# Kernel optimization log

Hardware: AMD Instinct MI355X
Metric: run time of the kernel (lower is better)

## Reference

```python
import jax, jax.numpy as jnp
import numpy as np

B, S, D = 2, 2048, 1024
H, HD = 16, 64
WINDOW = 256
THETA = 10000.0
SCALING = 1.0


def _rope_tables(seq_len, dim, dtype):
    # Matches RotaryEmbedding: inv_freq over even indices, emb = cat((freqs, freqs), -1)
    inv_freq = 1.0 / (THETA ** (jnp.arange(0, dim, 2, dtype=jnp.float32) / dim))
    t = jnp.arange(seq_len, dtype=jnp.float32) / max(SCALING, 1e-6)
    freqs = jnp.outer(t, inv_freq)                      # [S, HD/2]
    emb = jnp.concatenate((freqs, freqs), axis=-1)      # [S, HD]
    return jnp.cos(emb).astype(dtype), jnp.sin(emb).astype(dtype)


def _rotate_half(x):
    # interleaved-pair rotation, faithful to the torch code
    x1 = x[..., ::2]
    x2 = x[..., 1::2]
    return jnp.stack((-x2, x1), axis=-1).reshape(x.shape)


def setup_inputs() -> dict:
    key = jax.random.key(0)
    ks = jax.random.split(key, 5)
    x = jax.random.normal(ks[0], (B, S, D), dtype=jnp.float32)
    w = lambda k: (jax.random.normal(k, (D, D), dtype=jnp.float32) * 0.02)
    return {"x": x, "Wq": w(ks[1]), "Wk": w(ks[2]), "Wv": w(ks[3]), "Wo": w(ks[4])}


def reference(x, Wq, Wk, Wv, Wo):
    bsz, seq_len, d_model = x.shape
    # QKV projections (torch Linear: y = x @ W.T), reshape to [B, H, S, HD]
    def proj(W):
        return (x @ W.T).reshape(bsz, seq_len, H, HD).transpose(0, 2, 1, 3)
    q, k, v = proj(Wq), proj(Wk), proj(Wv)

    cos, sin = _rope_tables(seq_len, HD, x.dtype)       # [S, HD]
    cos = cos[None, None]                               # [1,1,S,HD]
    sin = sin[None, None]
    q = q * cos + _rotate_half(q) * sin
    k = k * cos + _rotate_half(k) * sin

    scale = 1.0 / jnp.sqrt(jnp.asarray(HD, dtype=x.dtype))
    scores = jnp.einsum('bhqd,bhkd->bhqk', q, k) * scale  # [B,H,S,S]

    idx = jnp.arange(seq_len)
    allow = (idx[:, None] >= idx[None, :]) & (idx[:, None] - idx[None, :] < WINDOW)
    neg = jnp.asarray(jnp.finfo(scores.dtype).min, dtype=scores.dtype)
    scores = jnp.where(allow[None, None], scores, neg)

    attn = jax.nn.softmax(scores, axis=-1)
    y = jnp.einsum('bhqk,bhkd->bhqd', attn, v)           # [B,H,S,HD]
    y = y.transpose(0, 2, 1, 3).reshape(bsz, seq_len, d_model)
    return y @ Wo.T
```

## Files before the change

### kernel.cpp

```cpp
#include <hip/hip_runtime.h>
#include <math.h>
#include <stdint.h>

typedef unsigned short u16;
typedef __bf16 bf16x8 __attribute__((ext_vector_type(8)));
typedef float f32x4 __attribute__((ext_vector_type(4)));

constexpr int Bb = 2, Ss = 2048, Dd = 1024, Hh = 16, Hd = 64, Win = 256;
constexpr int Mtot = Bb * Ss;

__device__ __forceinline__ u16 f2bf(float f) {
    uint32_t u = __float_as_uint(f);
    u += 0x7fff + ((u >> 16) & 1);
    return (u16)(u >> 16);
}

__device__ __forceinline__ void gload16(const void* g, void* l) {
    __builtin_amdgcn_global_load_lds(
        (const __attribute__((address_space(1))) uint32_t*)g,
        (__attribute__((address_space(3))) uint32_t*)l, 16, 0, 0);
}

__global__ void prep(const float* __restrict__ x,
                     const float* __restrict__ Wq, const float* __restrict__ Wk,
                     const float* __restrict__ Wv, const float* __restrict__ Wo,
                     u16* __restrict__ xb,
                     u16* __restrict__ wqb, u16* __restrict__ wkb,
                     u16* __restrict__ wvb, u16* __restrict__ wob,
                     float2* __restrict__ cs) {
    const int bid = blockIdx.x;
    if (bid < 8192) {
        const float* s;
        u16* d;
        int i;
        if (bid < 4096) {
            s = x; d = xb; i = bid * 256 + threadIdx.x;
        } else {
            int wsel = (bid - 4096) >> 10;
            i = ((bid - 4096) & 1023) * 256 + threadIdx.x;
            s = (wsel == 0) ? Wq : (wsel == 1) ? Wk : (wsel == 2) ? Wv : Wo;
            d = (wsel == 0) ? wqb : (wsel == 1) ? wkb : (wsel == 2) ? wvb : wob;
        }
        float4 v = reinterpret_cast<const float4*>(s)[i];
        ushort4 o;
        o.x = f2bf(v.x); o.y = f2bf(v.y); o.z = f2bf(v.z); o.w = f2bf(v.w);
        reinterpret_cast<ushort4*>(d)[i] = o;
    } else {
        int i = (bid - 8192) * 256 + threadIdx.x;
        int s = i >> 6, d = i & 63;
        float invf = powf(10000.0f, -(float)(d & 31) / 32.0f);
        float ang = (float)s * invf;
        float2 c; c.x = cosf(ang); c.y = sinf(ang);
        cs[i] = c;
    }
}

template <int MODE>
__global__ __launch_bounds__(512) void gemm_k(
    const u16* __restrict__ A,
    const u16* __restrict__ B0, const u16* __restrict__ B1, const u16* __restrict__ B2,
    void* __restrict__ C0, void* __restrict__ C1, void* __restrict__ C2,
    const float2* __restrict__ cs,
    int M, int N, int Kd)
{
    const int z = blockIdx.z;
    const u16* Am;
    const u16* Bm;
    int m0, n0;
    if (MODE == 0 && z == 2) {
        Am = B2; Bm = A;
        m0 = blockIdx.y * 128;
        n0 = blockIdx.x * 128;
    } else {
        Am = A;
        Bm = (z == 0) ? B0 : (z == 1) ? B1 : B2;
        m0 = blockIdx.x * 128;
        n0 = blockIdx.y * 128;
    }
    void* C = (z == 0) ? C0 : (z == 1) ? C1 : C2;

    __shared__ u16 sA[128 * 64];
    __shared__ u16 sB[128 * 64];

    const int t = threadIdx.x, l = t & 63, w = t >> 6;
    const int wm = w >> 2, wn = w & 3;
    const int lr = l & 15, kg = l >> 4;

    f32x4 acc[4][2] = {};

    for (int k0 = 0; k0 < Kd; k0 += 64) {
        __syncthreads();
#pragma unroll
        for (int p = 0; p < 2; ++p) {
            int i = p * 512 + t;
            int r = i >> 3;
            int gg = (i & 7) ^ (r & 7);
            gload16(Am + (size_t)(m0 + r) * Kd + k0 + gg * 8, &sA[i * 8]);
            gload16(Bm + (size_t)(n0 + r) * Kd + k0 + gg * 8, &sB[i * 8]);
        }
        __syncthreads();

        bf16x8 af[4][2], bfr[2][2];
#pragma unroll
        for (int im = 0; im < 4; ++im) {
            int r = wm * 64 + im * 16 + lr;
#pragma unroll
            for (int ks = 0; ks < 2; ++ks) {
                int slot = (ks * 4 + kg) ^ (r & 7);
                af[im][ks] = *reinterpret_cast<const bf16x8*>(&sA[r * 64 + slot * 8]);
            }
        }
#pragma unroll
        for (int in = 0; in < 2; ++in) {
            int r = wn * 32 + in * 16 + lr;
#pragma unroll
            for (int ks = 0; ks < 2; ++ks) {
                int slot = (ks * 4 + kg) ^ (r & 7);
                bfr[in][ks] = *reinterpret_cast<const bf16x8*>(&sB[r * 64 + slot * 8]);
            }
        }
#pragma unroll
        for (int im = 0; im < 4; ++im)
#pragma unroll
            for (int in = 0; in < 2; ++in) {
                acc[im][in] = __builtin_amdgcn_mfma_f32_16x16x32_bf16(
                    af[im][0], bfr[in][0], acc[im][in], 0, 0, 0);
                acc[im][in] = __builtin_amdgcn_mfma_f32_16x16x32_bf16(
                    af[im][1], bfr[in][1], acc[im][in], 0, 0, 0);
            }
    }

#pragma unroll
    for (int im = 0; im < 4; ++im) {
#pragma unroll
        for (int in = 0; in < 2; ++in) {
#pragma unroll
            for (int j = 0; j < 4; ++j) {
                int row = m0 + wm * 64 + im * 16 + kg * 4 + j;
                int col = n0 + wn * 32 + in * 16 + lr;
                float v = acc[im][in][j];
                if (MODE == 0) {
                    if (z == 2) {
                        int h = row >> 6, d = row & 63;
                        int b = col >> 11, s = col & 2047;
                        ((u16*)C)[((size_t)((b * 16 + h) * 64 + d)) * 2048 + s] = f2bf(v);
                    } else {
                        float vp = __shfl_xor(v, 1);
                        int b = row >> 11, s = row & 2047;
                        int h = col >> 6, d = col & 63;
                        float2 c2 = cs[s * 64 + d];
                        float outv = (col & 1) ? (v * c2.x + vp * c2.y)
                                               : (v * c2.x - vp * c2.y);
                        ((u16*)C)[(((size_t)(b * 16 + h)) * 2048 + s) * 64 + d] = f2bf(outv);
                    }
                } else {
                    ((float*)C)[(size_t)row * N + col] = v;
                }
            }
        }
    }
}

__global__ __launch_bounds__(256) void fattn(
    const u16* __restrict__ Qb, const u16* __restrict__ Kb,
    const u16* __restrict__ Vt, u16* __restrict__ O)
{
    __shared__ u16 sQ[64 * 64];
    __shared__ u16 sK[64 * 64];
    __shared__ u16 sVT[64 * 64];
    __shared__ u16 sP[4][16 * 64];

    const int t = threadIdx.x, l = t & 63, w = t >> 6;
    const int lo = l & 15, hi = l >> 4;
    const int qt = blockIdx.x, bh = blockIdx.y;
    const int q0 = qt * 64;

    const char* Qg = (const char*)(Qb + ((size_t)bh * Ss + q0) * 64);
#pragma unroll
    for (int p = 0; p < 2; ++p) {
        uint32_t x = (uint32_t)(w * 2 + p) * 1024 + l * 16;
        uint32_t sx = x ^ (((x >> 7) & 7) << 4);
        gload16(Qg + sx, (char*)sQ + x);
    }
    __syncthreads();

    bf16x8 qf[2];
#pragma unroll
    for (int ck = 0; ck < 2; ++ck) {
        uint32_t b = (uint32_t)(w * 16 + lo) * 128 + ck * 64 + hi * 16;
        b ^= ((lo & 7) << 4);
        qf[ck] = *reinterpret_cast<const bf16x8*>((const char*)sQ + b);
    }

    f32x4 o[4] = {};
    float mj[4], lj[4];
#pragma unroll
    for (int j = 0; j < 4; ++j) { mj[j] = -1e30f; lj[j] = 0.f; }

    const int jt0 = (qt >= 4) ? qt - 4 : 0;
    for (int jt = jt0; jt <= qt; ++jt) {
        __syncthreads();
        const char* Kg = (const char*)(Kb + ((size_t)bh * Ss + jt * 64) * 64);
#pragma unroll
        for (int p = 0; p < 2; ++p) {
            uint32_t x = (uint32_t)(w * 2 + p) * 1024 + l * 16;
            uint32_t sx = x ^ (((x >> 7) & 7) << 4);
            gload16(Kg + sx, (char*)sK + x);
        }
        const char* Vg = (const char*)(Vt + (size_t)bh * 64 * 2048 + (size_t)jt * 64);
#pragma unroll
        for (int p = 0; p < 2; ++p) {
            uint32_t x = (uint32_t)(w * 2 + p) * 1024 + l * 16;
            uint32_t sx = x ^ (((x >> 7) & 7) << 4);
            gload16(Vg + (size_t)(x >> 7) * 4096 + (sx & 127), (char*)sVT + x);
        }
        __syncthreads();

        f32x4 s4[4] = {};
#pragma unroll
        for (int ck = 0; ck < 2; ++ck) {
#pragma unroll
            for (int nb = 0; nb < 4; ++nb) {
                uint32_t b = (uint32_t)(nb * 16 + lo) * 128 + ck * 64 + hi * 16;
                b ^= ((lo & 7) << 4);
                bf16x8 kf = *reinterpret_cast<const bf16x8*>((const char*)sK + b);
                s4[nb] = __builtin_amdgcn_mfma_f32_16x16x32_bf16(qf[ck], kf, s4[nb], 0, 0, 0);
            }
        }

        const int qbase = q0 + w * 16 + hi * 4;
#pragma unroll
        for (int nb = 0; nb < 4; ++nb) {
            int k = jt * 64 + nb * 16 + lo;
#pragma unroll
            for (int j = 0; j < 4; ++j) {
                int q = qbase + j;
                float v = s4[nb][j] * 0.125f;
                bool ok = (k <= q) && (q - k < Win);
                s4[nb][j] = ok ? v : -1e30f;
            }
        }

#pragma unroll
        for (int j = 0; j < 4; ++j) {
            float tm = fmaxf(fmaxf(s4[0][j], s4[1][j]), fmaxf(s4[2][j], s4[3][j]));
            tm = fmaxf(tm, __shfl_xor(tm, 1));
            tm = fmaxf(tm, __shfl_xor(tm, 2));
            tm = fmaxf(tm, __shfl_xor(tm, 4));
            tm = fmaxf(tm, __shfl_xor(tm, 8));
            float nm = fmaxf(fmaxf(mj[j], tm), -1e20f);
            float sc = __expf(mj[j] - nm);
            mj[j] = nm;
            lj[j] *= sc;
#pragma unroll
            for (int nb = 0; nb < 4; ++nb) o[nb][j] *= sc;
            float ps = 0.f;
#pragma unroll
            for (int nb = 0; nb < 4; ++nb) {
                float p = __expf(s4[nb][j] - nm);
                ps += p;
                s4[nb][j] = p;
            }
            lj[j] += ps;
        }

#pragma unroll
        for (int nb = 0; nb < 4; ++nb) {
#pragma unroll
            for (int j = 0; j < 4; ++j) {
                int r = hi * 4 + j;
                uint32_t b = ((uint32_t)r * 128 + (nb * 16 + lo) * 2) ^ (((uint32_t)(r & 7)) << 4);
                *(u16*)((char*)&sP[w][0] + b) = f2bf(s4[nb][j]);
            }
        }

#pragma unroll
        for (int ck = 0; ck < 2; ++ck) {
            uint32_t bp = ((uint32_t)lo * 128 + ck * 64 + hi * 16) ^ (((uint32_t)(lo & 7)) << 4);
            bf16x8 pa = *reinterpret_cast<const bf16x8*>((const char*)&sP[w][0] + bp);
#pragma unroll
            for (int nb = 0; nb < 4; ++nb) {
                uint32_t bb = ((uint32_t)(nb * 16 + lo) * 128 + ck * 64 + hi * 16) ^ (((uint32_t)(lo & 7)) << 4);
                bf16x8 vf = *reinterpret_cast<const bf16x8*>((const char*)sVT + bb);
                o[nb] = __builtin_amdgcn_mfma_f32_16x16x32_bf16(pa, vf, o[nb], 0, 0, 0);
            }
        }
    }

#pragma unroll
    for (int j = 0; j < 4; ++j) {
        float s = lj[j];
        s += __shfl_xor(s, 1);
        s += __shfl_xor(s, 2);
        s += __shfl_xor(s, 4);
        s += __shfl_xor(s, 8);
        lj[j] = 1.0f / s;
    }
    const int bq = bh >> 4, h = bh & 15;
#pragma unroll
    for (int nb = 0; nb < 4; ++nb) {
#pragma unroll
        for (int j = 0; j < 4; ++j) {
            int q = q0 + w * 16 + hi * 4 + j;
            int d = nb * 16 + lo;
            O[((size_t)(bq * Ss + q)) * Dd + h * 64 + d] = f2bf(o[nb][j] * lj[j]);
        }
    }
}

extern "C" void kernel_launch(void* const* d_in, const int* in_sizes, int n_in,
                              void* d_out, int out_size, void* d_ws, size_t ws_size,
                              hipStream_t stream) {
    const float* x  = (const float*)d_in[0];
    const float* Wq = (const float*)d_in[1];
    const float* Wk = (const float*)d_in[2];
    const float* Wv = (const float*)d_in[3];
    const float* Wo = (const float*)d_in[4];
    float* out = (float*)d_out;

    char* ws = (char*)d_ws;
    size_t off = 0;
    auto carve = [&](size_t bytes) -> char* {
        char* p = ws + off;
        off += (bytes + 255) & ~(size_t)255;
        return p;
    };
    float2* cs = (float2*)carve((size_t)Ss * 64 * 8);
    u16* xb  = (u16*)carve((size_t)Mtot * Dd * 2);
    u16* wqb = (u16*)carve((size_t)Dd * Dd * 2);
    u16* wkb = (u16*)carve((size_t)Dd * Dd * 2);
    u16* wvb = (u16*)carve((size_t)Dd * Dd * 2);
    u16* wob = (u16*)carve((size_t)Dd * Dd * 2);
    u16* Qbb = (u16*)carve((size_t)Mtot * Dd * 2);
    u16* Kbb = (u16*)carve((size_t)Mtot * Dd * 2);
    u16* Vtb = (u16*)carve((size_t)Mtot * Dd * 2);
    u16* attb = (u16*)carve((size_t)Mtot * Dd * 2);

    prep<<<8704, 256, 0, stream>>>(x, Wq, Wk, Wv, Wo,
                                   xb, wqb, wkb, wvb, wob, cs);

    gemm_k<0><<<dim3(Mtot / 128, Dd / 128, 3), 512, 0, stream>>>(
        xb, wqb, wkb, wvb, Qbb, Kbb, Vtb, cs, Mtot, Dd, Dd);

    fattn<<<dim3(Ss / 64, Bb * Hh), 256, 0, stream>>>(Qbb, Kbb, Vtb, attb);

    gemm_k<1><<<dim3(Mtot / 128, Dd / 128, 1), 512, 0, stream>>>(
        attb, wob, wob, wob, out, out, out, nullptr, Mtot, Dd, Dd);
}
```

Measured before the change: 91.64 us.

## Load Q, K, V fragments directly from global memory instead of staging in LDS

The attention kernel no longer stages the Q, K and V^T tiles in shared memory through async global-to-LDS loads. Each wave now reads its MFMA operand fragments straight from global memory, which also removes the two block-wide barriers per key tile. The goal is to cut LDS traffic and synchronisation stalls. In exchange, all four waves fetch the same K/V data through the cache instead of sharing one staged copy, so there are more redundant global loads and latency with no prefetch overlap.

New measurement: 116.8 us. +27.5%, slower.

```diff
diff --git a/kernel.cpp b/kernel.cpp
--- a/kernel.cpp
+++ b/kernel.cpp
@@ -165,9 +165,6 @@
     const u16* __restrict__ Qb, const u16* __restrict__ Kb,
     const u16* __restrict__ Vt, u16* __restrict__ O)
 {
-    __shared__ u16 sQ[64 * 64];
-    __shared__ u16 sK[64 * 64];
-    __shared__ u16 sVT[64 * 64];
     __shared__ u16 sP[4][16 * 64];
 
     const int t = threadIdx.x, l = t & 63, w = t >> 6;
@@ -175,21 +172,12 @@
     const int qt = blockIdx.x, bh = blockIdx.y;
     const int q0 = qt * 64;
 
-    const char* Qg = (const char*)(Qb + ((size_t)bh * Ss + q0) * 64);
-#pragma unroll
-    for (int p = 0; p < 2; ++p) {
-        uint32_t x = (uint32_t)(w * 2 + p) * 1024 + l * 16;
-        uint32_t sx = x ^ (((x >> 7) & 7) << 4);
-        gload16(Qg + sx, (char*)sQ + x);
-    }
-    __syncthreads();
-
     bf16x8 qf[2];
-#pragma unroll
-    for (int ck = 0; ck < 2; ++ck) {
-        uint32_t b = (uint32_t)(w * 16 + lo) * 128 + ck * 64 + hi * 16;
-        b ^= ((lo & 7) << 4);
-        qf[ck] = *reinterpret_cast<const bf16x8*>((const char*)sQ + b);
+    {
+        const u16* Qr = Qb + ((size_t)bh * Ss + q0 + w * 16 + lo) * 64 + hi * 8;
+#pragma unroll
+        for (int ck = 0; ck < 2; ++ck)
+            qf[ck] = *reinterpret_cast<const bf16x8*>(Qr + ck * 32);
     }
 
     f32x4 o[4] = {};
@@ -197,33 +185,18 @@
 #pragma unroll
     for (int j = 0; j < 4; ++j) { mj[j] = -1e30f; lj[j] = 0.f; }
 
+    const u16* Kg = Kb + (size_t)bh * Ss * 64;
+    const u16* Vg = Vt + (size_t)bh * 64 * 2048;
+
     const int jt0 = (qt >= 4) ? qt - 4 : 0;
     for (int jt = jt0; jt <= qt; ++jt) {
-        __syncthreads();
-        const char* Kg = (const char*)(Kb + ((size_t)bh * Ss + jt * 64) * 64);
-#pragma unroll
-        for (int p = 0; p < 2; ++p) {
-            uint32_t x = (uint32_t)(w * 2 + p) * 1024 + l * 16;
-            uint32_t sx = x ^ (((x >> 7) & 7) << 4);
-            gload16(Kg + sx, (char*)sK + x);
-        }
-        const char* Vg = (const char*)(Vt + (size_t)bh * 64 * 2048 + (size_t)jt * 64);
-#pragma unroll
-        for (int p = 0; p < 2; ++p) {
-            uint32_t x = (uint32_t)(w * 2 + p) * 1024 + l * 16;
-            uint32_t sx = x ^ (((x >> 7) & 7) << 4);
-            gload16(Vg + (size_t)(x >> 7) * 4096 + (sx & 127), (char*)sVT + x);
-        }
-        __syncthreads();
-
         f32x4 s4[4] = {};
 #pragma unroll
         for (int ck = 0; ck < 2; ++ck) {
 #pragma unroll
             for (int nb = 0; nb < 4; ++nb) {
-                uint32_t b = (uint32_t)(nb * 16 + lo) * 128 + ck * 64 + hi * 16;
-                b ^= ((lo & 7) << 4);
-                bf16x8 kf = *reinterpret_cast<const bf16x8*>((const char*)sK + b);
+                bf16x8 kf = *reinterpret_cast<const bf16x8*>(
+                    Kg + (size_t)(jt * 64 + nb * 16 + lo) * 64 + ck * 32 + hi * 8);
                 s4[nb] = __builtin_amdgcn_mfma_f32_16x16x32_bf16(qf[ck], kf, s4[nb], 0, 0, 0);
             }
         }
@@ -280,8 +253,8 @@
             bf16x8 pa = *reinterpret_cast<const bf16x8*>((const char*)&sP[w][0] + bp);
 #pragma unroll
             for (int nb = 0; nb < 4; ++nb) {
-                uint32_t bb = ((uint32_t)(nb * 16 + lo) * 128 + ck * 64 + hi * 16) ^ (((uint32_t)(lo & 7)) << 4);
-                bf16x8 vf = *reinterpret_cast<const bf16x8*>((const char*)sVT + bb);
+                bf16x8 vf = *reinterpret_cast<const bf16x8*>(
+                    Vg + (size_t)(nb * 16 + lo) * 2048 + jt * 64 + ck * 32 + hi * 8);
                 o[nb] = __builtin_amdgcn_mfma_f32_16x16x32_bf16(pa, vf, o[nb], 0, 0, 0);
             }
         }
```
